# Kernel tuning notes

Measured on AMD Instinct MI355X. Metric: run time of the kernel, lower is better.

## Reference

```python
import jax, jax.numpy as jnp
import numpy as np

EMB_SIZE = 768
NUM_HEADS = 8


def setup_inputs() -> dict:
    key = jax.random.key(0)
    ks = jax.random.split(key, 6)
    B, N, E = 8, 1024, EMB_SIZE
    return {
        "x": jax.random.normal(ks[0], (B, N, E), dtype=jnp.float32),
        "relative_pos": jax.random.normal(ks[1], (NUM_HEADS, N, N), dtype=jnp.float32),
        "qkv_w": jax.random.normal(ks[2], (2 * E, E), dtype=jnp.float32) * 0.02,
        "qkv_b": jax.random.normal(ks[3], (2 * E,), dtype=jnp.float32) * 0.02,
        "val_w": jax.random.normal(ks[4], (E, E), dtype=jnp.float32) * 0.02,
        "val_b": jax.random.normal(ks[5], (E,), dtype=jnp.float32) * 0.02,
    }


def reference(x, relative_pos, qkv_w, qkv_b, val_w, val_b):
    B, N, E = x.shape
    H = NUM_HEADS
    D = E // H
    # qkv projection: [B, N, 2E]; last dim layout is (h, d, qk) per einops rearrange
    qkv = (x @ qkv_w.T + qkv_b).reshape(B, N, H, D, 2)
    q = jnp.transpose(qkv[..., 0], (0, 2, 1, 3))  # [B, H, N, D]
    k = jnp.transpose(qkv[..., 1], (0, 2, 1, 3))  # [B, H, N, D]
    scale = E ** 0.5  # original divides by sqrt(emb_size), not sqrt(d_head)
    energy = jnp.einsum('bhqd,bhkd->bhqk', q, k) / scale  # [B, H, N, N]
    # relative_pos [H, N, N] broadcasts over batch
    energy = jax.nn.softmax(energy + relative_pos, axis=-1)
    values = x @ val_w.T + val_b  # [B, N, E]
    return values, energy
```

## Files before the change

### kernel.cpp

```cpp
#include <hip/hip_runtime.h>
#include <hip/hip_bf16.h>

#define EMB 768
#define NH 8
#define DH 96
#define BATCH 8
#define SEQ 1024
#define M_TOT (BATCH * SEQ)
#define NCOLS (3 * EMB)

typedef float f32x4 __attribute__((ext_vector_type(4)));
typedef __bf16 bf16x8 __attribute__((ext_vector_type(8)));

__device__ __forceinline__ unsigned short f2bf_bits(float f) {
  __hip_bfloat16 b = __float2bfloat16(f);
  return *reinterpret_cast<unsigned short*>(&b);
}

__device__ __forceinline__ void gload_lds16(const void* g, void* l) {
  __builtin_amdgcn_global_load_lds(
      (__attribute__((address_space(1))) void*)(g),
      (__attribute__((address_space(3))) void*)(l), 16, 0, 0);
}

__global__ void prep_x_kernel(const float* __restrict__ x, __hip_bfloat16* __restrict__ xb) {
  const int n4 = M_TOT * EMB / 4;
  int i = blockIdx.x * blockDim.x + threadIdx.x;
  if (i < n4) {
    f32x4 v = reinterpret_cast<const f32x4*>(x)[i];
    ushort4 o;
    o.x = f2bf_bits(v[0]);
    o.y = f2bf_bits(v[1]);
    o.z = f2bf_bits(v[2]);
    o.w = f2bf_bits(v[3]);
    reinterpret_cast<ushort4*>(xb)[i] = o;
  }
}

__global__ void prep_w_kernel(const float* __restrict__ qkv_w, const float* __restrict__ qkv_b,
                              const float* __restrict__ val_w, const float* __restrict__ val_b,
                              __hip_bfloat16* __restrict__ Wall, float* __restrict__ bias) {
  const float inv_s = 0.03608439182435161f;
  int idx = blockIdx.x * 256 + threadIdx.x;
  if (idx >= NCOLS * EMB) return;
  int r = idx / EMB;
  int c = idx - r * EMB;
  float v;
  if (r < EMB) {
    int h = r / DH, d = r - h * DH;
    int src = h * 192 + 2 * d;
    v = qkv_w[(size_t)src * EMB + c] * inv_s;
    if (c == 0) bias[r] = qkv_b[src] * inv_s;
  } else if (r < 2 * EMB) {
    int r2 = r - EMB;
    int h = r2 / DH, d = r2 - h * DH;
    int src = h * 192 + 2 * d + 1;
    v = qkv_w[(size_t)src * EMB + c];
    if (c == 0) bias[r] = qkv_b[src];
  } else {
    int r3 = r - 2 * EMB;
    v = val_w[(size_t)r3 * EMB + c];
    if (c == 0) bias[r] = val_b[r3];
  }
  Wall[idx] = __float2bfloat16(v);
}

__global__ __launch_bounds__(256) void gemm_kernel(
    const __hip_bfloat16* __restrict__ xb, const __hip_bfloat16* __restrict__ Wall,
    const float* __restrict__ bias, __hip_bfloat16* __restrict__ qhead,
    __hip_bfloat16* __restrict__ khead, float* __restrict__ vout) {
  __shared__ __hip_bfloat16 As[128 * 32];
  __shared__ __hip_bfloat16 Bs[128 * 32];
  const int tid = threadIdx.x;
  const int w = tid >> 6, l = tid & 63;
  const int m0 = blockIdx.x * 128;
  const int n0 = blockIdx.y * 128;
  const int wr = w >> 1, wc = w & 1;

  f32x4 acc[4][4] = {};

  const int sr0 = (w * 2 + 0) * 16 + (l >> 2);
  const int sr1 = (w * 2 + 1) * 16 + (l >> 2);
  const int sc = (l & 3) * 8;

  for (int kt = 0; kt < EMB / 32; ++kt) {
    const int k0 = kt * 32;
    gload_lds16(xb + (size_t)(m0 + sr0) * EMB + k0 + sc, (void*)(As + (w * 2 + 0) * 512));
    gload_lds16(xb + (size_t)(m0 + sr1) * EMB + k0 + sc, (void*)(As + (w * 2 + 1) * 512));
    gload_lds16(Wall + (size_t)(n0 + sr0) * EMB + k0 + sc, (void*)(Bs + (w * 2 + 0) * 512));
    gload_lds16(Wall + (size_t)(n0 + sr1) * EMB + k0 + sc, (void*)(Bs + (w * 2 + 1) * 512));
    __syncthreads();

    bf16x8 af[4], bfr[4];
#pragma unroll
    for (int t = 0; t < 4; ++t) {
      af[t] = *reinterpret_cast<const bf16x8*>(As + (wr * 64 + t * 16 + (l & 15)) * 32 + (l >> 4) * 8);
      bfr[t] = *reinterpret_cast<const bf16x8*>(Bs + (wc * 64 + t * 16 + (l & 15)) * 32 + (l >> 4) * 8);
    }
#pragma unroll
    for (int i = 0; i < 4; ++i)
#pragma unroll
      for (int j = 0; j < 4; ++j)
        acc[i][j] = __builtin_amdgcn_mfma_f32_16x16x32_bf16(af[i], bfr[j], acc[i][j], 0, 0, 0);
    __syncthreads();
  }

  const int rowbase = m0 + wr * 64;
  const int colbase = n0 + wc * 64;
#pragma unroll
  for (int j = 0; j < 4; ++j) {
    const int n = colbase + j * 16 + (l & 15);
    const float bb = bias[n];
#pragma unroll
    for (int i = 0; i < 4; ++i) {
#pragma unroll
      for (int q = 0; q < 4; ++q) {
        const int m = rowbase + i * 16 + (l >> 4) * 4 + q;
        const float v = acc[i][j][q] + bb;
        if (n0 >= 2 * EMB) {
          vout[(size_t)m * EMB + (n - 2 * EMB)] = v;
        } else {
          const int nn = (n0 >= EMB) ? (n - EMB) : n;
          const int hh = nn / DH, dd = nn - hh * DH;
          const size_t off = ((size_t)((m >> 10) * NH + hh) * SEQ + (m & 1023)) * DH + dd;
          if (n0 >= EMB) khead[off] = __float2bfloat16(v);
          else qhead[off] = __float2bfloat16(v);
        }
      }
    }
  }
}

__global__ __launch_bounds__(512, 4) void attn_kernel(
    const __hip_bfloat16* __restrict__ qhead, const __hip_bfloat16* __restrict__ khead,
    const float* __restrict__ rel, float* __restrict__ eout) {
  __shared__ alignas(16) char smem[65536];
  __shared__ float redm[16][8];
  __shared__ float reds[16][8];
  __hip_bfloat16* Kb = (__hip_bfloat16*)smem;
  float* rel_lds = (float*)(smem + 24576);
  __hip_bfloat16* qlds = (__hip_bfloat16*)(smem + 33024);
  float* Sb = (float*)smem;

  const int t = threadIdx.x;
  const int w = t >> 6, l = t & 63;
  const int lr = l >> 4, lc = l & 15;
  const int flat = blockIdx.x;
  const int u = flat >> 6;
  const int b = (flat >> 3) & 7;
  const int g = u * 8 + (flat & 7);
  const int h = g >> 6;
  const int rb = g & 63;
  const int row0 = rb * 16;
  const int rowt = t >> 5, st = t & 31;

  const __hip_bfloat16* qsrc = qhead + ((size_t)(b * NH + h) * SEQ + row0) * DH;
  if (t < 192) gload_lds16(qsrc + t * 8, smem + 33024 + w * 1024);
  __syncthreads();

  bf16x8 qf[3];
#pragma unroll
  for (int kc = 0; kc < 3; ++kc)
    qf[kc] = *reinterpret_cast<const bf16x8*>(qlds + lc * DH + kc * 32 + lr * 8);

  const __hip_bfloat16* ksrc = khead + (size_t)(b * NH + h) * SEQ * DH;
  const float* relsrc = rel + ((size_t)h * SEQ + row0 + rowt) * SEQ + st * 4;

  f32x4 relreg = *reinterpret_cast<const f32x4*>(relsrc);
  f32x4 acc[8];

#pragma unroll
  for (int c = 0; c < 8; ++c) {
#pragma unroll
    for (int r = 0; r < 3; ++r)
      gload_lds16(ksrc + (size_t)c * 12288 + r * 4096 + t * 8, smem + r * 8192 + w * 1024);
    *reinterpret_cast<f32x4*>(rel_lds + rowt * 132 + st * 4) = relreg;
    __syncthreads();
    if (c < 7) relreg = *reinterpret_cast<const f32x4*>(relsrc + (size_t)(c + 1) * 128);
    f32x4 a = {0.f, 0.f, 0.f, 0.f};
    __builtin_amdgcn_s_setprio(1);
#pragma unroll
    for (int kc = 0; kc < 3; ++kc) {
      bf16x8 kf = *reinterpret_cast<const bf16x8*>(Kb + (w * 16 + lc) * DH + kc * 32 + lr * 8);
      a = __builtin_amdgcn_mfma_f32_16x16x32_bf16(kf, qf[kc], a, 0, 0, 0);
    }
    __builtin_amdgcn_s_setprio(0);
    a = a + *reinterpret_cast<const f32x4*>(rel_lds + lc * 132 + w * 16 + lr * 4);
    acc[c] = a;
    __syncthreads();
  }

  float mx = -3.4e38f;
#pragma unroll
  for (int c = 0; c < 8; ++c)
    mx = fmaxf(mx, fmaxf(fmaxf(acc[c][0], acc[c][1]), fmaxf(acc[c][2], acc[c][3])));
  mx = fmaxf(mx, __shfl_xor(mx, 16));
  mx = fmaxf(mx, __shfl_xor(mx, 32));
  if (l < 16) redm[lc][w] = mx;
  __syncthreads();
  float M = redm[lc][0];
#pragma unroll
  for (int i = 1; i < 8; ++i) M = fmaxf(M, redm[lc][i]);

  float sm = 0.f;
#pragma unroll
  for (int c = 0; c < 8; ++c) {
#pragma unroll
    for (int j = 0; j < 4; ++j) {
      float e = __expf(acc[c][j] - M);
      acc[c][j] = e;
      sm += e;
    }
  }
  sm += __shfl_xor(sm, 16);
  sm += __shfl_xor(sm, 32);
  if (l < 16) reds[lc][w] = sm;
  __syncthreads();
  float S = 0.f;
#pragma unroll
  for (int i = 0; i < 8; ++i) S += reds[lc][i];
  const float rinv = 1.0f / S;

#pragma unroll
  for (int c = 0; c < 8; ++c) {
    f32x4 v = acc[c] * rinv;
    const int col = c * 128 + w * 16 + lr * 4;
    *reinterpret_cast<f32x4*>(Sb + lc * 1024 + (col ^ ((lc & 7) << 2))) = v;
  }
  __syncthreads();
  float* ebase = eout + ((size_t)(b * NH + h) * SEQ + row0 + rowt) * SEQ;
#pragma unroll
  for (int p = 0; p < 8; ++p) {
    const int col = p * 128 + st * 4;
    f32x4 v = *reinterpret_cast<const f32x4*>(Sb + rowt * 1024 + (col ^ ((rowt & 7) << 2)));
    *reinterpret_cast<f32x4*>(ebase + col) = v;
  }
}

extern "C" void kernel_launch(void* const* d_in, const int* in_sizes, int n_in,
                              void* d_out, int out_size, void* d_ws, size_t ws_size,
                              hipStream_t stream) {
  const float* x = (const float*)d_in[0];
  const float* rel = (const float*)d_in[1];
  const float* qkv_w = (const float*)d_in[2];
  const float* qkv_b = (const float*)d_in[3];
  const float* val_w = (const float*)d_in[4];
  const float* val_b = (const float*)d_in[5];
  float* out = (float*)d_out;

  char* ws = (char*)d_ws;
  __hip_bfloat16* xb = (__hip_bfloat16*)(ws);
  __hip_bfloat16* Wall = (__hip_bfloat16*)(ws + 12582912);
  float* bias = (float*)(ws + 16121856);
  __hip_bfloat16* qhead = (__hip_bfloat16*)(ws + 16131072);
  __hip_bfloat16* khead = (__hip_bfloat16*)(ws + 28713984);

  float* vout = out;
  float* eout = out + (size_t)M_TOT * EMB;

  prep_x_kernel<<<dim3(M_TOT * EMB / 4 / 256), dim3(256), 0, stream>>>(x, xb);
  prep_w_kernel<<<dim3(NCOLS * EMB / 256), dim3(256), 0, stream>>>(qkv_w, qkv_b, val_w, val_b,
                                                                   Wall, bias);
  gemm_kernel<<<dim3(M_TOT / 128, NCOLS / 128), dim3(256), 0, stream>>>(xb, Wall, bias, qhead,
                                                                        khead, vout);
  attn_kernel<<<dim3(SEQ / 16 * NH * BATCH), dim3(512), 0, stream>>>(qhead, khead, rel, eout);
}
```

Before: 190.1 us.

## Double-buffer per-wave K tiles and drop LDS staging for rel and output

Each wave now stages only its own 16 K rows into a private double-buffered LDS slice with async global-to-LDS loads, waiting on vmcnt instead of block-wide barriers in the score loop. Q and the relative-position bias are read straight from global into registers, and the softmax output is written directly from MFMA layout to global rather than being transposed through LDS. This removes most __syncthreads and LDS round trips, at the cost of less coalesced 64-byte-segment global reads and writes for rel and the energy output.

```diff
diff --git a/kernel.cpp b/kernel.cpp
--- a/kernel.cpp
+++ b/kernel.cpp
@@ -134,13 +134,9 @@
 __global__ __launch_bounds__(512, 4) void attn_kernel(
     const __hip_bfloat16* __restrict__ qhead, const __hip_bfloat16* __restrict__ khead,
     const float* __restrict__ rel, float* __restrict__ eout) {
-  __shared__ alignas(16) char smem[65536];
+  __shared__ alignas(16) char KS[49152];
   __shared__ float redm[16][8];
   __shared__ float reds[16][8];
-  __hip_bfloat16* Kb = (__hip_bfloat16*)smem;
-  float* rel_lds = (float*)(smem + 24576);
-  __hip_bfloat16* qlds = (__hip_bfloat16*)(smem + 33024);
-  float* Sb = (float*)smem;
 
   const int t = threadIdx.x;
   const int w = t >> 6, l = t & 63;
@@ -152,43 +148,51 @@
   const int h = g >> 6;
   const int rb = g & 63;
   const int row0 = rb * 16;
-  const int rowt = t >> 5, st = t & 31;
-
-  const __hip_bfloat16* qsrc = qhead + ((size_t)(b * NH + h) * SEQ + row0) * DH;
-  if (t < 192) gload_lds16(qsrc + t * 8, smem + 33024 + w * 1024);
-  __syncthreads();
-
+
+  const __hip_bfloat16* qsrc = qhead + ((size_t)(b * NH + h) * SEQ + row0 + lc) * DH;
   bf16x8 qf[3];
 #pragma unroll
   for (int kc = 0; kc < 3; ++kc)
-    qf[kc] = *reinterpret_cast<const bf16x8*>(qlds + lc * DH + kc * 32 + lr * 8);
-
-  const __hip_bfloat16* ksrc = khead + (size_t)(b * NH + h) * SEQ * DH;
-  const float* relsrc = rel + ((size_t)h * SEQ + row0 + rowt) * SEQ + st * 4;
-
-  f32x4 relreg = *reinterpret_cast<const f32x4*>(relsrc);
+    qf[kc] = *reinterpret_cast<const bf16x8*>(qsrc + kc * 32 + lr * 8);
+
+  const __hip_bfloat16* ksrc =
+      khead + (size_t)(b * NH + h) * SEQ * DH + (size_t)w * 16 * DH;
+  char* kdst = KS + w * 6144;
+
+#define STAGE_K(c, buf)                                                             \
+  {                                                                                 \
+    const __hip_bfloat16* s_ = ksrc + (size_t)(c) * 12288 + (size_t)l * 8;          \
+    gload_lds16(s_, kdst + (buf) * 3072);                                           \
+    gload_lds16(s_ + 512, kdst + (buf) * 3072 + 1024);                              \
+    gload_lds16(s_ + 1024, kdst + (buf) * 3072 + 2048);                             \
+  }
+
+  STAGE_K(0, 0)
+
+  const float* relsrc = rel + ((size_t)h * SEQ + row0 + lc) * SEQ + w * 16 + lr * 4;
   f32x4 acc[8];
 
 #pragma unroll
   for (int c = 0; c < 8; ++c) {
-#pragma unroll
-    for (int r = 0; r < 3; ++r)
-      gload_lds16(ksrc + (size_t)c * 12288 + r * 4096 + t * 8, smem + r * 8192 + w * 1024);
-    *reinterpret_cast<f32x4*>(rel_lds + rowt * 132 + st * 4) = relreg;
-    __syncthreads();
-    if (c < 7) relreg = *reinterpret_cast<const f32x4*>(relsrc + (size_t)(c + 1) * 128);
+    f32x4 relv = *reinterpret_cast<const f32x4*>(relsrc + c * 128);
+    if (c < 7) STAGE_K(c + 1, (c + 1) & 1)
+    if (c < 7) {
+      asm volatile("s_waitcnt vmcnt(4)" ::: "memory");
+    } else {
+      asm volatile("s_waitcnt vmcnt(1)" ::: "memory");
+    }
+    __builtin_amdgcn_sched_barrier(0);
+    const __hip_bfloat16* kp =
+        reinterpret_cast<const __hip_bfloat16*>(kdst + (c & 1) * 3072) + lc * DH;
     f32x4 a = {0.f, 0.f, 0.f, 0.f};
-    __builtin_amdgcn_s_setprio(1);
 #pragma unroll
     for (int kc = 0; kc < 3; ++kc) {
-      bf16x8 kf = *reinterpret_cast<const bf16x8*>(Kb + (w * 16 + lc) * DH + kc * 32 + lr * 8);
+      bf16x8 kf = *reinterpret_cast<const bf16x8*>(kp + kc * 32 + lr * 8);
       a = __builtin_amdgcn_mfma_f32_16x16x32_bf16(kf, qf[kc], a, 0, 0, 0);
     }
-    __builtin_amdgcn_s_setprio(0);
-    a = a + *reinterpret_cast<const f32x4*>(rel_lds + lc * 132 + w * 16 + lr * 4);
-    acc[c] = a;
-    __syncthreads();
-  }
+    acc[c] = a + relv;
+  }
+#undef STAGE_K
 
   float mx = -3.4e38f;
 #pragma unroll
@@ -221,19 +225,11 @@
   for (int i = 0; i < 8; ++i) S += reds[lc][i];
   const float rinv = 1.0f / S;
 
+  float* op = eout + ((size_t)(b * NH + h) * SEQ + row0 + lc) * SEQ + w * 16 + lr * 4;
 #pragma unroll
   for (int c = 0; c < 8; ++c) {
     f32x4 v = acc[c] * rinv;
-    const int col = c * 128 + w * 16 + lr * 4;
-    *reinterpret_cast<f32x4*>(Sb + lc * 1024 + (col ^ ((lc & 7) << 2))) = v;
-  }
-  __syncthreads();
-  float* ebase = eout + ((size_t)(b * NH + h) * SEQ + row0 + rowt) * SEQ;
-#pragma unroll
-  for (int p = 0; p < 8; ++p) {
-    const int col = p * 128 + st * 4;
-    f32x4 v = *reinterpret_cast<const f32x4*>(Sb + rowt * 1024 + (col ^ ((rowt & 7) << 2)));
-    *reinterpret_cast<f32x4*>(ebase + col) = v;
+    *reinterpret_cast<f32x4*>(op + c * 128) = v;
   }
 }
 
```

New measurement: 197.3 us. 3.8% more time.
